# Performance work log

Hardware: AMD Instinct MI355X
Metric: run time of the kernel (lower is better)

## Reference

```python
import jax, jax.numpy as jnp
import numpy as np

KSIZE = 3  # module init kwarg


def setup_inputs() -> dict:
    key = jax.random.key(0)
    k1, k2, k3 = jax.random.split(key, 3)
    shape = (16, 3, 512, 512)  # [B, C, H, W]
    return {
        "sr": jax.random.normal(k1, shape, jnp.float32),
        "sr_ema": jax.random.normal(k2, shape, jnp.float32),
        "hr": jax.random.normal(k3, shape, jnp.float32),
    }


def _local_var(res, ksize):
    """Unbiased variance over a ksize x ksize sliding window with reflect pad.

    Matches torch: reflect-pad then unfold + var(unbiased=True). Implemented as a
    box-filter over sum and sum-of-squares (no ksize^2-larger unfold tensor).
    res: [B, 1, H, W] -> [B, 1, H, W]
    """
    pad = (ksize - 1) // 2
    rp = jnp.pad(res, ((0, 0), (0, 0), (pad, pad), (pad, pad)), mode="reflect")
    n = ksize * ksize
    win = (1, 1, ksize, ksize)
    strides = (1, 1, 1, 1)
    zero = jnp.zeros((), rp.dtype)
    s = jax.lax.reduce_window(rp, zero, jax.lax.add, win, strides, "VALID")
    sq = jax.lax.reduce_window(rp * rp, zero, jax.lax.add, win, strides, "VALID")
    # unbiased: (sum(x^2) - sum(x)^2/n) / (n-1)
    return (sq - s * s / n) / (n - 1)


def reference(sr, sr_ema, hr):
    # per-pixel channel-summed residuals, [B, 1, H, W]
    residual_ema = jnp.sum(jnp.abs(hr - sr_ema), axis=1, keepdims=True) / 255.0
    residual_sr = jnp.sum(jnp.abs(hr - sr), axis=1, keepdims=True) / 255.0

    r_det = jax.lax.stop_gradient(residual_sr)  # .clone().detach() in torch

    # patch-level weight: unbiased var over (C=1, H, W) per sample, ** (1/5)
    n_patch = r_det.shape[1] * r_det.shape[2] * r_det.shape[3]
    mean = jnp.mean(r_det, axis=(-1, -2, -3), keepdims=True)
    patch_var = jnp.sum((r_det - mean) ** 2, axis=(-1, -2, -3), keepdims=True) / (n_patch - 1)
    patch_w = patch_var ** 0.2  # [B,1,1,1]

    pixel_w = _local_var(r_det, KSIZE)  # [B,1,H,W]

    overall_w = patch_w * pixel_w
    overall_w = jnp.where(residual_sr < residual_ema, jnp.zeros((), overall_w.dtype), overall_w)

    # L1 loss (mean reduction) between weighted sr and weighted hr
    return jnp.mean(jnp.abs(overall_w * sr - overall_w * hr))
```

## Files before the change

kernel.cpp:

```cpp
#include <hip/hip_runtime.h>
#include <math.h>


#define BB 16
#define HH 512
#define WW 512
#define HW (HH * WW)
#define CHW (3 * HW)
#define TILES_PER_BATCH 64
#define NBLOCKS (BB * TILES_PER_BATCH)
#define LDS_STRIDE 264

__device__ __forceinline__ int reflect_h(int gh) {
  gh = gh < 0 ? -gh : gh;
  return gh >= HH ? 2 * HH - 2 - gh : gh;
}

__global__ __launch_bounds__(256, 4) void wl1_main(
    const float* __restrict__ sr, const float* __restrict__ srema,
    const float* __restrict__ hr,
    float* __restrict__ p_sum, float* __restrict__ p_sum2,
    float* __restrict__ p_loss) {
  __shared__ float rt[18][LDS_STRIDE];
  const int bid = blockIdx.x;
  const int b = bid >> 6;
  const int t = bid & 63;
  const int h0 = (t >> 1) << 4;
  const int w0 = (t & 1) << 8;
  const int tid = threadIdx.x;
  const int c4 = tid & 63;
  const int rs = tid >> 6;
  const float* __restrict__ srb = sr + (size_t)b * CHW;
  const float* __restrict__ hrb = hr + (size_t)b * CHW;
  const float* __restrict__ eb = srema + (size_t)b * CHW;

  if (tid < 36) {
    int row = tid >> 1, side = tid & 1;
    int gh = reflect_h(h0 - 1 + row);
    int gw = side ? w0 + 256 : w0 - 1;
    if (gw < 0) gw = 1;
    if (gw > 511) gw = 1022 - gw;
    int base = gh * WW + gw;
    float v = (fabsf(hrb[base] - srb[base]) +
               fabsf(hrb[base + HW] - srb[base + HW]) +
               fabsf(hrb[base + 2 * HW] - srb[base + 2 * HW])) /
              255.0f;
    rt[row][side ? 260 : 3] = v;
  }

  float e_r[4][4];
#pragma unroll
  for (int it = 0; it < 5; ++it) {
    const int row = 4 * it + rs;
    if (row < 18) {
      const int gh = reflect_h(h0 - 1 + row);
      const float* hb = hrb + gh * WW + w0 + 4 * c4;
      const float* sb = srb + gh * WW + w0 + 4 * c4;
      float4 ha = *(const float4*)(hb);
      float4 hbv = *(const float4*)(hb + HW);
      float4 hc = *(const float4*)(hb + 2 * HW);
      float4 sa = *(const float4*)(sb);
      float4 sbv = *(const float4*)(sb + HW);
      float4 sc = *(const float4*)(sb + 2 * HW);
      const bool do_e = (row >= 1) && (row <= 16);
      float4 ea, eb2, ec;
      if (do_e) {
        const float* ep = eb + gh * WW + w0 + 4 * c4;
        ea = *(const float4*)(ep);
        eb2 = *(const float4*)(ep + HW);
        ec = *(const float4*)(ep + 2 * HW);
      }
      float4 r4;
      r4.x = (fabsf(ha.x - sa.x) + fabsf(hbv.x - sbv.x) + fabsf(hc.x - sc.x)) / 255.0f;
      r4.y = (fabsf(ha.y - sa.y) + fabsf(hbv.y - sbv.y) + fabsf(hc.y - sc.y)) / 255.0f;
      r4.z = (fabsf(ha.z - sa.z) + fabsf(hbv.z - sbv.z) + fabsf(hc.z - sc.z)) / 255.0f;
      r4.w = (fabsf(ha.w - sa.w) + fabsf(hbv.w - sbv.w) + fabsf(hc.w - sc.w)) / 255.0f;
      *(float4*)&rt[row][4 + 4 * c4] = r4;
      if (do_e) {
        e_r[it & 3][0] = (fabsf(ha.x - ea.x) + fabsf(hbv.x - eb2.x) + fabsf(hc.x - ec.x)) / 255.0f;
        e_r[it & 3][1] = (fabsf(ha.y - ea.y) + fabsf(hbv.y - eb2.y) + fabsf(hc.y - ec.y)) / 255.0f;
        e_r[it & 3][2] = (fabsf(ha.z - ea.z) + fabsf(hbv.z - eb2.z) + fabsf(hc.z - ec.z)) / 255.0f;
        e_r[it & 3][3] = (fabsf(ha.w - ea.w) + fabsf(hbv.w - eb2.w) + fabsf(hc.w - ec.w)) / 255.0f;
      }
    }
  }
  __syncthreads();

  float v1 = 0.f, v2 = 0.f, v3 = 0.f;
#pragma unroll
  for (int it = 0; it < 5; ++it) {
    const int row = 4 * it + rs;
    if (row >= 1 && row <= 16) {
      const int o = row - 1;
      float cs[6] = {0, 0, 0, 0, 0, 0}, cq[6] = {0, 0, 0, 0, 0, 0};
      float center[4];
#pragma unroll
      for (int dr = 0; dr < 3; ++dr) {
        const float* lp = &rt[o + dr][4 * c4];
        float4 a = *(const float4*)(lp);
        float4 bq = *(const float4*)(lp + 4);
        float4 cq4 = *(const float4*)(lp + 8);
        float f3 = a.w, f4 = bq.x, f5 = bq.y, f6 = bq.z, f7 = bq.w, f8 = cq4.x;
        cs[0] += f3; cq[0] += f3 * f3;
        cs[1] += f4; cq[1] += f4 * f4;
        cs[2] += f5; cq[2] += f5 * f5;
        cs[3] += f6; cq[3] += f6 * f6;
        cs[4] += f7; cq[4] += f7 * f7;
        cs[5] += f8; cq[5] += f8 * f8;
        if (dr == 1) { center[0] = f4; center[1] = f5; center[2] = f6; center[3] = f7; }
      }
#pragma unroll
      for (int cc = 0; cc < 4; ++cc) {
        float s = cs[cc] + cs[cc + 1] + cs[cc + 2];
        float q = cq[cc] + cq[cc + 1] + cq[cc + 2];
        float pvar = (q - s * s / 9.0f) / 8.0f;
        float rc = center[cc];
        v1 += rc;
        v2 += rc * rc;
        if (rc >= e_r[it & 3][cc]) v3 += pvar * (255.0f * rc);
      }
    }
  }

#pragma unroll
  for (int off = 32; off > 0; off >>= 1) {
    v1 += __shfl_down(v1, off, 64);
    v2 += __shfl_down(v2, off, 64);
    v3 += __shfl_down(v3, off, 64);
  }
  __shared__ float red[3][4];
  if (c4 == 0) {
    red[0][rs] = v1;
    red[1][rs] = v2;
    red[2][rs] = v3;
  }
  __syncthreads();
  if (tid == 0) {
    p_sum[bid] = red[0][0] + red[0][1] + red[0][2] + red[0][3];
    p_sum2[bid] = red[1][0] + red[1][1] + red[1][2] + red[1][3];
    p_loss[bid] = red[2][0] + red[2][1] + red[2][2] + red[2][3];
  }
}

__global__ __launch_bounds__(1024) void wl1_reduce(
    const float* __restrict__ p_sum, const float* __restrict__ p_sum2,
    const float* __restrict__ p_loss, float* __restrict__ out) {
  const int tid = threadIdx.x;
  const int b = tid >> 6, k = tid & 63;
  const int i = b * TILES_PER_BATCH + k;
  double s = (double)p_sum[i], s2 = (double)p_sum2[i], sl = (double)p_loss[i];
#pragma unroll
  for (int off = 32; off > 0; off >>= 1) {
    s += __shfl_down(s, off, 64);
    s2 += __shfl_down(s2, off, 64);
    sl += __shfl_down(sl, off, 64);
  }
  __shared__ double acc[BB];
  if (k == 0) {
    const double n = (double)HW;
    double var = (s2 - s * s / n) / (n - 1.0);
    acc[b] = pow(var, 0.2) * sl;
  }
  __syncthreads();
  if (tid == 0) {
    double tot = 0.0;
#pragma unroll
    for (int j = 0; j < BB; ++j) tot += acc[j];
    out[0] = (float)(tot / (double)((size_t)BB * CHW));
  }
}

extern "C" void kernel_launch(void* const* d_in, const int* in_sizes, int n_in,
                              void* d_out, int out_size, void* d_ws,
                              size_t ws_size, hipStream_t stream) {
  const float* sr = (const float*)d_in[0];
  const float* srema = (const float*)d_in[1];
  const float* hr = (const float*)d_in[2];
  float* out = (float*)d_out;

  float* p_sum = (float*)d_ws;
  float* p_sum2 = p_sum + NBLOCKS;
  float* p_loss = p_sum2 + NBLOCKS;

  wl1_main<<<NBLOCKS, 256, 0, stream>>>(sr, srema, hr, p_sum, p_sum2, p_loss);
  wl1_reduce<<<1, 1024, 0, stream>>>(p_sum, p_sum2, p_loss, out);
}
```

Baseline: 167.8 us.

## Replace LDS tile with per-wave register rolling window over row strips

Each wave now processes an 8-row, 256-column strip, streaming rows through registers with a prefetched next row and a rolling three-row window of box-filter partial sums. Horizontal neighbours come from lane shuffles, so the shared-memory tile and its block barrier are gone. Halo reread overhead rises (2 extra rows per 8 instead of per 16), and register pressure grows, which is why launch bounds drop to two blocks per CU. The reduce kernel is adjusted for 32 blocks per batch.

```diff
diff --git a/kernel.cpp b/kernel.cpp
--- a/kernel.cpp
+++ b/kernel.cpp
@@ -7,119 +7,145 @@
 #define WW 512
 #define HW (HH * WW)
 #define CHW (3 * HW)
-#define TILES_PER_BATCH 64
-#define NBLOCKS (BB * TILES_PER_BATCH)
-#define LDS_STRIDE 264
+#define SH 8
+#define STRIPS (HH / SH)
+#define BLOCKS_PER_BATCH ((STRIPS * 2) / 4)
+#define NBLOCKS (BB * BLOCKS_PER_BATCH)
 
 __device__ __forceinline__ int reflect_h(int gh) {
   gh = gh < 0 ? -gh : gh;
   return gh >= HH ? 2 * HH - 2 - gh : gh;
 }
 
-__global__ __launch_bounds__(256, 4) void wl1_main(
+struct Row {
+  float4 h0, h1, h2, s0, s1, s2, m0, m1, m2;
+  float eh0, eh1, eh2, es0, es1, es2;
+};
+
+__device__ __forceinline__ Row load_row(const float* __restrict__ hrb,
+                                        const float* __restrict__ srb,
+                                        const float* __restrict__ emb,
+                                        int gh, int col, bool isEdge, int gwE,
+                                        bool with_e) {
+  Row r;
+  const int base = gh * WW + col;
+  r.h0 = *(const float4*)(hrb + base);
+  r.h1 = *(const float4*)(hrb + base + HW);
+  r.h2 = *(const float4*)(hrb + base + 2 * HW);
+  r.s0 = *(const float4*)(srb + base);
+  r.s1 = *(const float4*)(srb + base + HW);
+  r.s2 = *(const float4*)(srb + base + 2 * HW);
+  if (with_e) {
+    r.m0 = *(const float4*)(emb + base);
+    r.m1 = *(const float4*)(emb + base + HW);
+    r.m2 = *(const float4*)(emb + base + 2 * HW);
+  }
+  if (isEdge) {
+    const int be = gh * WW + gwE;
+    r.eh0 = hrb[be];
+    r.eh1 = hrb[be + HW];
+    r.eh2 = hrb[be + 2 * HW];
+    r.es0 = srb[be];
+    r.es1 = srb[be + HW];
+    r.es2 = srb[be + 2 * HW];
+  }
+  return r;
+}
+
+__global__ __launch_bounds__(256, 2) void wl1_main(
     const float* __restrict__ sr, const float* __restrict__ srema,
     const float* __restrict__ hr,
     float* __restrict__ p_sum, float* __restrict__ p_sum2,
     float* __restrict__ p_loss) {
-  __shared__ float rt[18][LDS_STRIDE];
+  const int tid = threadIdx.x;
+  const int wv = tid >> 6;
+  const int lane = tid & 63;
   const int bid = blockIdx.x;
-  const int b = bid >> 6;
-  const int t = bid & 63;
-  const int h0 = (t >> 1) << 4;
-  const int w0 = (t & 1) << 8;
-  const int tid = threadIdx.x;
-  const int c4 = tid & 63;
-  const int rs = tid >> 6;
+  const int b = bid >> 5;
+  const int slot = ((bid & 31) << 2) | wv;
+  const int r0 = (slot >> 1) * SH;
+  const int w0 = (slot & 1) << 8;
+  const int col = w0 + 4 * lane;
+  const bool isEdge = (lane == 0) || (lane == 63);
+  const int gwE = (lane == 0) ? (w0 ? w0 - 1 : 1)
+                              : (w0 + 256 < WW ? w0 + 256 : 2 * WW - 2 - (w0 + 256));
   const float* __restrict__ srb = sr + (size_t)b * CHW;
   const float* __restrict__ hrb = hr + (size_t)b * CHW;
-  const float* __restrict__ eb = srema + (size_t)b * CHW;
-
-  if (tid < 36) {
-    int row = tid >> 1, side = tid & 1;
-    int gh = reflect_h(h0 - 1 + row);
-    int gw = side ? w0 + 256 : w0 - 1;
-    if (gw < 0) gw = 1;
-    if (gw > 511) gw = 1022 - gw;
-    int base = gh * WW + gw;
-    float v = (fabsf(hrb[base] - srb[base]) +
-               fabsf(hrb[base + HW] - srb[base + HW]) +
-               fabsf(hrb[base + 2 * HW] - srb[base + 2 * HW])) /
-              255.0f;
-    rt[row][side ? 260 : 3] = v;
-  }
-
-  float e_r[4][4];
-#pragma unroll
-  for (int it = 0; it < 5; ++it) {
-    const int row = 4 * it + rs;
-    if (row < 18) {
-      const int gh = reflect_h(h0 - 1 + row);
-      const float* hb = hrb + gh * WW + w0 + 4 * c4;
-      const float* sb = srb + gh * WW + w0 + 4 * c4;
-      float4 ha = *(const float4*)(hb);
-      float4 hbv = *(const float4*)(hb + HW);
-      float4 hc = *(const float4*)(hb + 2 * HW);
-      float4 sa = *(const float4*)(sb);
-      float4 sbv = *(const float4*)(sb + HW);
-      float4 sc = *(const float4*)(sb + 2 * HW);
-      const bool do_e = (row >= 1) && (row <= 16);
-      float4 ea, eb2, ec;
-      if (do_e) {
-        const float* ep = eb + gh * WW + w0 + 4 * c4;
-        ea = *(const float4*)(ep);
-        eb2 = *(const float4*)(ep + HW);
-        ec = *(const float4*)(ep + 2 * HW);
-      }
-      float4 r4;
-      r4.x = (fabsf(ha.x - sa.x) + fabsf(hbv.x - sbv.x) + fabsf(hc.x - sc.x)) / 255.0f;
-      r4.y = (fabsf(ha.y - sa.y) + fabsf(hbv.y - sbv.y) + fabsf(hc.y - sc.y)) / 255.0f;
-      r4.z = (fabsf(ha.z - sa.z) + fabsf(hbv.z - sbv.z) + fabsf(hc.z - sc.z)) / 255.0f;
-      r4.w = (fabsf(ha.w - sa.w) + fabsf(hbv.w - sbv.w) + fabsf(hc.w - sc.w)) / 255.0f;
-      *(float4*)&rt[row][4 + 4 * c4] = r4;
-      if (do_e) {
-        e_r[it & 3][0] = (fabsf(ha.x - ea.x) + fabsf(hbv.x - eb2.x) + fabsf(hc.x - ec.x)) / 255.0f;
-        e_r[it & 3][1] = (fabsf(ha.y - ea.y) + fabsf(hbv.y - eb2.y) + fabsf(hc.y - ec.y)) / 255.0f;
-        e_r[it & 3][2] = (fabsf(ha.z - ea.z) + fabsf(hbv.z - eb2.z) + fabsf(hc.z - ec.z)) / 255.0f;
-        e_r[it & 3][3] = (fabsf(ha.w - ea.w) + fabsf(hbv.w - eb2.w) + fabsf(hc.w - ec.w)) / 255.0f;
-      }
-    }
-  }
-  __syncthreads();
-
+  const float* __restrict__ emb = srema + (size_t)b * CHW;
+
+  float hA[4] = {0, 0, 0, 0}, qA[4] = {0, 0, 0, 0};
+  float hB[4] = {0, 0, 0, 0}, qB[4] = {0, 0, 0, 0};
+  float cB[4] = {0, 0, 0, 0}, eB[4] = {0, 0, 0, 0};
   float v1 = 0.f, v2 = 0.f, v3 = 0.f;
-#pragma unroll
-  for (int it = 0; it < 5; ++it) {
-    const int row = 4 * it + rs;
-    if (row >= 1 && row <= 16) {
-      const int o = row - 1;
-      float cs[6] = {0, 0, 0, 0, 0, 0}, cq[6] = {0, 0, 0, 0, 0, 0};
-      float center[4];
-#pragma unroll
-      for (int dr = 0; dr < 3; ++dr) {
-        const float* lp = &rt[o + dr][4 * c4];
-        float4 a = *(const float4*)(lp);
-        float4 bq = *(const float4*)(lp + 4);
-        float4 cq4 = *(const float4*)(lp + 8);
-        float f3 = a.w, f4 = bq.x, f5 = bq.y, f6 = bq.z, f7 = bq.w, f8 = cq4.x;
-        cs[0] += f3; cq[0] += f3 * f3;
-        cs[1] += f4; cq[1] += f4 * f4;
-        cs[2] += f5; cq[2] += f5 * f5;
-        cs[3] += f6; cq[3] += f6 * f6;
-        cs[4] += f7; cq[4] += f7 * f7;
-        cs[5] += f8; cq[5] += f8 * f8;
-        if (dr == 1) { center[0] = f4; center[1] = f5; center[2] = f6; center[3] = f7; }
-      }
+
+  Row cur = load_row(hrb, srb, emb, reflect_h(r0 - 1), col, isEdge, gwE, false);
+#pragma unroll
+  for (int st = 0; st <= SH + 1; ++st) {
+    Row nxt;
+    if (st <= SH) {
+      const int gh1 = (st == SH) ? reflect_h(r0 + SH) : (r0 + st);
+      nxt = load_row(hrb, srb, emb, gh1, col, isEdge, gwE, st < SH);
+    }
+    float4 r4;
+    r4.x = (fabsf(cur.h0.x - cur.s0.x) + fabsf(cur.h1.x - cur.s1.x) +
+            fabsf(cur.h2.x - cur.s2.x)) / 255.0f;
+    r4.y = (fabsf(cur.h0.y - cur.s0.y) + fabsf(cur.h1.y - cur.s1.y) +
+            fabsf(cur.h2.y - cur.s2.y)) / 255.0f;
+    r4.z = (fabsf(cur.h0.z - cur.s0.z) + fabsf(cur.h1.z - cur.s1.z) +
+            fabsf(cur.h2.z - cur.s2.z)) / 255.0f;
+    r4.w = (fabsf(cur.h0.w - cur.s0.w) + fabsf(cur.h1.w - cur.s1.w) +
+            fabsf(cur.h2.w - cur.s2.w)) / 255.0f;
+    float redge = 0.f;
+    if (isEdge)
+      redge = (fabsf(cur.eh0 - cur.es0) + fabsf(cur.eh1 - cur.es1) +
+               fabsf(cur.eh2 - cur.es2)) / 255.0f;
+    const float fl = __shfl_up(r4.w, 1, 64);
+    const float fr = __shfl_down(r4.x, 1, 64);
+    const float f3 = (lane == 0) ? redge : fl;
+    const float f8 = (lane == 63) ? redge : fr;
+    const float f0 = f3, f1v = r4.x, f2v = r4.y, f3v = r4.z, f4v = r4.w, f5v = f8;
+    float hC[4], qC[4];
+    hC[0] = f0 + f1v + f2v;
+    hC[1] = f1v + f2v + f3v;
+    hC[2] = f2v + f3v + f4v;
+    hC[3] = f3v + f4v + f5v;
+    qC[0] = f0 * f0 + f1v * f1v + f2v * f2v;
+    qC[1] = f1v * f1v + f2v * f2v + f3v * f3v;
+    qC[2] = f2v * f2v + f3v * f3v + f4v * f4v;
+    qC[3] = f3v * f3v + f4v * f4v + f5v * f5v;
+    float e4[4] = {0, 0, 0, 0};
+    if (st >= 1 && st <= SH) {
+      e4[0] = (fabsf(cur.h0.x - cur.m0.x) + fabsf(cur.h1.x - cur.m1.x) +
+               fabsf(cur.h2.x - cur.m2.x)) / 255.0f;
+      e4[1] = (fabsf(cur.h0.y - cur.m0.y) + fabsf(cur.h1.y - cur.m1.y) +
+               fabsf(cur.h2.y - cur.m2.y)) / 255.0f;
+      e4[2] = (fabsf(cur.h0.z - cur.m0.z) + fabsf(cur.h1.z - cur.m1.z) +
+               fabsf(cur.h2.z - cur.m2.z)) / 255.0f;
+      e4[3] = (fabsf(cur.h0.w - cur.m0.w) + fabsf(cur.h1.w - cur.m1.w) +
+               fabsf(cur.h2.w - cur.m2.w)) / 255.0f;
+    }
+    if (st >= 2) {
 #pragma unroll
       for (int cc = 0; cc < 4; ++cc) {
-        float s = cs[cc] + cs[cc + 1] + cs[cc + 2];
-        float q = cq[cc] + cq[cc + 1] + cq[cc + 2];
-        float pvar = (q - s * s / 9.0f) / 8.0f;
-        float rc = center[cc];
+        const float s3 = hA[cc] + hB[cc] + hC[cc];
+        const float q3 = qA[cc] + qB[cc] + qC[cc];
+        const float pvar = (q3 - s3 * s3 / 9.0f) / 8.0f;
+        const float rc = cB[cc];
         v1 += rc;
         v2 += rc * rc;
-        if (rc >= e_r[it & 3][cc]) v3 += pvar * (255.0f * rc);
+        if (rc >= eB[cc]) v3 += pvar * (255.0f * rc);
       }
     }
+#pragma unroll
+    for (int cc = 0; cc < 4; ++cc) {
+      hA[cc] = hB[cc];
+      qA[cc] = qB[cc];
+      hB[cc] = hC[cc];
+      qB[cc] = qC[cc];
+    }
+    cB[0] = r4.x; cB[1] = r4.y; cB[2] = r4.z; cB[3] = r4.w;
+    eB[0] = e4[0]; eB[1] = e4[1]; eB[2] = e4[2]; eB[3] = e4[3];
+    cur = nxt;
   }
 
 #pragma unroll
@@ -129,10 +155,10 @@
     v3 += __shfl_down(v3, off, 64);
   }
   __shared__ float red[3][4];
-  if (c4 == 0) {
-    red[0][rs] = v1;
-    red[1][rs] = v2;
-    red[2][rs] = v3;
+  if (lane == 0) {
+    red[0][wv] = v1;
+    red[1][wv] = v2;
+    red[2][wv] = v3;
   }
   __syncthreads();
   if (tid == 0) {
@@ -147,8 +173,13 @@
     const float* __restrict__ p_loss, float* __restrict__ out) {
   const int tid = threadIdx.x;
   const int b = tid >> 6, k = tid & 63;
-  const int i = b * TILES_PER_BATCH + k;
-  double s = (double)p_sum[i], s2 = (double)p_sum2[i], sl = (double)p_loss[i];
+  double s = 0.0, s2 = 0.0, sl = 0.0;
+  if (k < BLOCKS_PER_BATCH) {
+    const int i = b * BLOCKS_PER_BATCH + k;
+    s = (double)p_sum[i];
+    s2 = (double)p_sum2[i];
+    sl = (double)p_loss[i];
+  }
 #pragma unroll
   for (int off = 32; off > 0; off >>= 1) {
     s += __shfl_down(s, off, 64);
```

New measurement: 172.3 us. 2.7% more time.

## Fuse final reduction into main kernel via last-block atomic counter

Applied to the files above, without the earlier changes.

Merges the separate reduction kernel into the main kernel: each block bumps an atomic counter after writing its partials, and the last block does the per-batch variance and final sum. The load phase is also restructured. Interior rows are loaded with full sr/sr_ema/hr and the ema residual is stashed in LDS, while the two halo rows go to 128 dedicated threads. Patch sums move into the load loop. The change removes one kernel launch and the register array, but adds a memset, an atomic with fences, and a dead leftover loop that sums partials nobody uses.

```diff
diff --git a/kernel.cpp b/kernel.cpp
--- a/kernel.cpp
+++ b/kernel.cpp
@@ -7,8 +7,7 @@
 #define WW 512
 #define HW (HH * WW)
 #define CHW (3 * HW)
-#define TILES_PER_BATCH 64
-#define NBLOCKS (BB * TILES_PER_BATCH)
+#define NT 1024
 #define LDS_STRIDE 264
 
 __device__ __forceinline__ int reflect_h(int gh) {
@@ -16,12 +15,14 @@
   return gh >= HH ? 2 * HH - 2 - gh : gh;
 }
 
-__global__ __launch_bounds__(256, 4) void wl1_main(
+__global__ __launch_bounds__(256) void wl1_fused(
     const float* __restrict__ sr, const float* __restrict__ srema,
     const float* __restrict__ hr,
     float* __restrict__ p_sum, float* __restrict__ p_sum2,
-    float* __restrict__ p_loss) {
+    float* __restrict__ p_loss, unsigned int* __restrict__ counter,
+    float* __restrict__ out) {
   __shared__ float rt[18][LDS_STRIDE];
+  __shared__ float ee[16][256];
   const int bid = blockIdx.x;
   const int b = bid >> 6;
   const int t = bid & 63;
@@ -32,93 +33,105 @@
   const int rs = tid >> 6;
   const float* __restrict__ srb = sr + (size_t)b * CHW;
   const float* __restrict__ hrb = hr + (size_t)b * CHW;
-  const float* __restrict__ eb = srema + (size_t)b * CHW;
-
-  if (tid < 36) {
-    int row = tid >> 1, side = tid & 1;
-    int gh = reflect_h(h0 - 1 + row);
+  const float* __restrict__ emb = srema + (size_t)b * CHW;
+
+  float v1 = 0.f, v2 = 0.f, v3 = 0.f;
+
+#pragma unroll
+  for (int k = 0; k < 4; ++k) {
+    const int o = 4 * k + rs;
+    const int base = (h0 + o) * WW + w0 + 4 * c4;
+    const float* hp = hrb + base;
+    const float* sp = srb + base;
+    const float* ep = emb + base;
+    float4 h0v = *(const float4*)(hp);
+    float4 h1v = *(const float4*)(hp + HW);
+    float4 h2v = *(const float4*)(hp + 2 * HW);
+    float4 s0v = *(const float4*)(sp);
+    float4 s1v = *(const float4*)(sp + HW);
+    float4 s2v = *(const float4*)(sp + 2 * HW);
+    float4 e0v = *(const float4*)(ep);
+    float4 e1v = *(const float4*)(ep + HW);
+    float4 e2v = *(const float4*)(ep + 2 * HW);
+    float4 r4;
+    r4.x = (fabsf(h0v.x - s0v.x) + fabsf(h1v.x - s1v.x) + fabsf(h2v.x - s2v.x)) / 255.0f;
+    r4.y = (fabsf(h0v.y - s0v.y) + fabsf(h1v.y - s1v.y) + fabsf(h2v.y - s2v.y)) / 255.0f;
+    r4.z = (fabsf(h0v.z - s0v.z) + fabsf(h1v.z - s1v.z) + fabsf(h2v.z - s2v.z)) / 255.0f;
+    r4.w = (fabsf(h0v.w - s0v.w) + fabsf(h1v.w - s1v.w) + fabsf(h2v.w - s2v.w)) / 255.0f;
+    float4 e4;
+    e4.x = (fabsf(h0v.x - e0v.x) + fabsf(h1v.x - e1v.x) + fabsf(h2v.x - e2v.x)) / 255.0f;
+    e4.y = (fabsf(h0v.y - e0v.y) + fabsf(h1v.y - e1v.y) + fabsf(h2v.y - e2v.y)) / 255.0f;
+    e4.z = (fabsf(h0v.z - e0v.z) + fabsf(h1v.z - e1v.z) + fabsf(h2v.z - e2v.z)) / 255.0f;
+    e4.w = (fabsf(h0v.w - e0v.w) + fabsf(h1v.w - e1v.w) + fabsf(h2v.w - e2v.w)) / 255.0f;
+    *(float4*)&rt[o + 1][4 + 4 * c4] = r4;
+    *(float4*)&ee[o][4 * c4] = e4;
+    v1 += r4.x + r4.y + r4.z + r4.w;
+    v2 += r4.x * r4.x + r4.y * r4.y + r4.z * r4.z + r4.w * r4.w;
+  }
+
+  if (tid < 128) {
+    const int row = (tid >> 6) * 17;
+    const int gh = reflect_h(h0 - 1 + row);
+    const int base = gh * WW + w0 + 4 * (tid & 63);
+    const float* hp = hrb + base;
+    const float* sp = srb + base;
+    float4 h0v = *(const float4*)(hp);
+    float4 h1v = *(const float4*)(hp + HW);
+    float4 h2v = *(const float4*)(hp + 2 * HW);
+    float4 s0v = *(const float4*)(sp);
+    float4 s1v = *(const float4*)(sp + HW);
+    float4 s2v = *(const float4*)(sp + 2 * HW);
+    float4 r4;
+    r4.x = (fabsf(h0v.x - s0v.x) + fabsf(h1v.x - s1v.x) + fabsf(h2v.x - s2v.x)) / 255.0f;
+    r4.y = (fabsf(h0v.y - s0v.y) + fabsf(h1v.y - s1v.y) + fabsf(h2v.y - s2v.y)) / 255.0f;
+    r4.z = (fabsf(h0v.z - s0v.z) + fabsf(h1v.z - s1v.z) + fabsf(h2v.z - s2v.z)) / 255.0f;
+    r4.w = (fabsf(h0v.w - s0v.w) + fabsf(h1v.w - s1v.w) + fabsf(h2v.w - s2v.w)) / 255.0f;
+    *(float4*)&rt[row][4 + 4 * (tid & 63)] = r4;
+  } else if (tid < 164) {
+    const int ht = tid - 128;
+    const int row = ht >> 1, side = ht & 1;
+    const int gh = reflect_h(h0 - 1 + row);
     int gw = side ? w0 + 256 : w0 - 1;
     if (gw < 0) gw = 1;
     if (gw > 511) gw = 1022 - gw;
-    int base = gh * WW + gw;
+    const int base = gh * WW + gw;
     float v = (fabsf(hrb[base] - srb[base]) +
                fabsf(hrb[base + HW] - srb[base + HW]) +
                fabsf(hrb[base + 2 * HW] - srb[base + 2 * HW])) /
               255.0f;
     rt[row][side ? 260 : 3] = v;
   }
-
-  float e_r[4][4];
-#pragma unroll
-  for (int it = 0; it < 5; ++it) {
-    const int row = 4 * it + rs;
-    if (row < 18) {
-      const int gh = reflect_h(h0 - 1 + row);
-      const float* hb = hrb + gh * WW + w0 + 4 * c4;
-      const float* sb = srb + gh * WW + w0 + 4 * c4;
-      float4 ha = *(const float4*)(hb);
-      float4 hbv = *(const float4*)(hb + HW);
-      float4 hc = *(const float4*)(hb + 2 * HW);
-      float4 sa = *(const float4*)(sb);
-      float4 sbv = *(const float4*)(sb + HW);
-      float4 sc = *(const float4*)(sb + 2 * HW);
-      const bool do_e = (row >= 1) && (row <= 16);
-      float4 ea, eb2, ec;
-      if (do_e) {
-        const float* ep = eb + gh * WW + w0 + 4 * c4;
-        ea = *(const float4*)(ep);
-        eb2 = *(const float4*)(ep + HW);
-        ec = *(const float4*)(ep + 2 * HW);
-      }
-      float4 r4;
-      r4.x = (fabsf(ha.x - sa.x) + fabsf(hbv.x - sbv.x) + fabsf(hc.x - sc.x)) / 255.0f;
-      r4.y = (fabsf(ha.y - sa.y) + fabsf(hbv.y - sbv.y) + fabsf(hc.y - sc.y)) / 255.0f;
-      r4.z = (fabsf(ha.z - sa.z) + fabsf(hbv.z - sbv.z) + fabsf(hc.z - sc.z)) / 255.0f;
-      r4.w = (fabsf(ha.w - sa.w) + fabsf(hbv.w - sbv.w) + fabsf(hc.w - sc.w)) / 255.0f;
-      *(float4*)&rt[row][4 + 4 * c4] = r4;
-      if (do_e) {
-        e_r[it & 3][0] = (fabsf(ha.x - ea.x) + fabsf(hbv.x - eb2.x) + fabsf(hc.x - ec.x)) / 255.0f;
-        e_r[it & 3][1] = (fabsf(ha.y - ea.y) + fabsf(hbv.y - eb2.y) + fabsf(hc.y - ec.y)) / 255.0f;
-        e_r[it & 3][2] = (fabsf(ha.z - ea.z) + fabsf(hbv.z - eb2.z) + fabsf(hc.z - ec.z)) / 255.0f;
-        e_r[it & 3][3] = (fabsf(ha.w - ea.w) + fabsf(hbv.w - eb2.w) + fabsf(hc.w - ec.w)) / 255.0f;
-      }
-    }
-  }
-  __syncthreads();
-
-  float v1 = 0.f, v2 = 0.f, v3 = 0.f;
-#pragma unroll
-  for (int it = 0; it < 5; ++it) {
-    const int row = 4 * it + rs;
-    if (row >= 1 && row <= 16) {
-      const int o = row - 1;
-      float cs[6] = {0, 0, 0, 0, 0, 0}, cq[6] = {0, 0, 0, 0, 0, 0};
-      float center[4];
-#pragma unroll
-      for (int dr = 0; dr < 3; ++dr) {
-        const float* lp = &rt[o + dr][4 * c4];
-        float4 a = *(const float4*)(lp);
-        float4 bq = *(const float4*)(lp + 4);
-        float4 cq4 = *(const float4*)(lp + 8);
-        float f3 = a.w, f4 = bq.x, f5 = bq.y, f6 = bq.z, f7 = bq.w, f8 = cq4.x;
-        cs[0] += f3; cq[0] += f3 * f3;
-        cs[1] += f4; cq[1] += f4 * f4;
-        cs[2] += f5; cq[2] += f5 * f5;
-        cs[3] += f6; cq[3] += f6 * f6;
-        cs[4] += f7; cq[4] += f7 * f7;
-        cs[5] += f8; cq[5] += f8 * f8;
-        if (dr == 1) { center[0] = f4; center[1] = f5; center[2] = f6; center[3] = f7; }
-      }
-#pragma unroll
-      for (int cc = 0; cc < 4; ++cc) {
-        float s = cs[cc] + cs[cc + 1] + cs[cc + 2];
-        float q = cq[cc] + cq[cc + 1] + cq[cc + 2];
-        float pvar = (q - s * s / 9.0f) / 8.0f;
-        float rc = center[cc];
-        v1 += rc;
-        v2 += rc * rc;
-        if (rc >= e_r[it & 3][cc]) v3 += pvar * (255.0f * rc);
-      }
+  __syncthreads();
+
+#pragma unroll
+  for (int rr = 0; rr < 4; ++rr) {
+    const int o = 4 * rr + rs;
+    float cs[6] = {0, 0, 0, 0, 0, 0}, cq[6] = {0, 0, 0, 0, 0, 0};
+    float center[4];
+#pragma unroll
+    for (int dr = 0; dr < 3; ++dr) {
+      const float* lp = &rt[o + dr][4 * c4];
+      float4 a = *(const float4*)(lp);
+      float4 bq = *(const float4*)(lp + 4);
+      float4 cq4 = *(const float4*)(lp + 8);
+      float f3 = a.w, f4 = bq.x, f5 = bq.y, f6 = bq.z, f7 = bq.w, f8 = cq4.x;
+      cs[0] += f3; cq[0] += f3 * f3;
+      cs[1] += f4; cq[1] += f4 * f4;
+      cs[2] += f5; cq[2] += f5 * f5;
+      cs[3] += f6; cq[3] += f6 * f6;
+      cs[4] += f7; cq[4] += f7 * f7;
+      cs[5] += f8; cq[5] += f8 * f8;
+      if (dr == 1) { center[0] = f4; center[1] = f5; center[2] = f6; center[3] = f7; }
+    }
+    const float4 e4 = *(const float4*)&ee[o][4 * c4];
+    const float ev[4] = {e4.x, e4.y, e4.z, e4.w};
+#pragma unroll
+    for (int cc = 0; cc < 4; ++cc) {
+      float s = cs[cc] + cs[cc + 1] + cs[cc + 2];
+      float q = cq[cc] + cq[cc + 1] + cq[cc + 2];
+      float pvar = (q - s * s / 9.0f) / 8.0f;
+      float rc = center[cc];
+      if (rc >= ev[cc]) v3 += pvar * (255.0f * rc);
     }
   }
 
@@ -135,37 +148,60 @@
     red[2][rs] = v3;
   }
   __syncthreads();
+  __shared__ int is_last;
   if (tid == 0) {
     p_sum[bid] = red[0][0] + red[0][1] + red[0][2] + red[0][3];
     p_sum2[bid] = red[1][0] + red[1][1] + red[1][2] + red[1][3];
     p_loss[bid] = red[2][0] + red[2][1] + red[2][2] + red[2][3];
-  }
-}
-
-__global__ __launch_bounds__(1024) void wl1_reduce(
-    const float* __restrict__ p_sum, const float* __restrict__ p_sum2,
-    const float* __restrict__ p_loss, float* __restrict__ out) {
-  const int tid = threadIdx.x;
-  const int b = tid >> 6, k = tid & 63;
-  const int i = b * TILES_PER_BATCH + k;
-  double s = (double)p_sum[i], s2 = (double)p_sum2[i], sl = (double)p_loss[i];
-#pragma unroll
-  for (int off = 32; off > 0; off >>= 1) {
-    s += __shfl_down(s, off, 64);
-    s2 += __shfl_down(s2, off, 64);
-    sl += __shfl_down(sl, off, 64);
-  }
-  __shared__ double acc[BB];
-  if (k == 0) {
-    const double n = (double)HW;
-    double var = (s2 - s * s / n) / (n - 1.0);
-    acc[b] = pow(var, 0.2) * sl;
+    __threadfence();
+    unsigned int prev = atomicAdd(counter, 1u);
+    is_last = (prev == NT - 1) ? 1 : 0;
+  }
+  __syncthreads();
+  if (is_last == 0) return;
+
+  __threadfence();
+  double s = 0.0, s2 = 0.0, sl = 0.0;
+#pragma unroll
+  for (int j = 0; j < 4; ++j) {
+    const int i = tid + 256 * j;
+    s += (double)p_sum[i];
+    s2 += (double)p_sum2[i];
+    sl += (double)p_loss[i];
+  }
+  __shared__ double bs[BB], bs2[BB], bsl[BB];
+  if (tid < BB) { bs[tid] = 0.0; bs2[tid] = 0.0; bsl[tid] = 0.0; }
+  __syncthreads();
+  if (tid < 64) {
+  }
+  if (tid < 128) {
+    const int bb = tid >> 3;
+    const int kk = tid & 7;
+    double ls = 0.0, ls2 = 0.0, lsl = 0.0;
+#pragma unroll
+    for (int j = 0; j < 8; ++j) {
+      const int i = (bb << 6) + (kk << 3) + j;
+      ls += (double)p_sum[i];
+      ls2 += (double)p_sum2[i];
+      lsl += (double)p_loss[i];
+    }
+#pragma unroll
+    for (int off = 4; off > 0; off >>= 1) {
+      ls += __shfl_down(ls, off, 64);
+      ls2 += __shfl_down(ls2, off, 64);
+      lsl += __shfl_down(lsl, off, 64);
+    }
+    if (kk == 0) {
+      const double n = (double)HW;
+      double var = (ls2 - ls * ls / n) / (n - 1.0);
+      bs[bb] = pow(var, 0.2) * lsl;
+    }
   }
   __syncthreads();
   if (tid == 0) {
     double tot = 0.0;
 #pragma unroll
-    for (int j = 0; j < BB; ++j) tot += acc[j];
+    for (int j = 0; j < BB; ++j) tot += bs[j];
     out[0] = (float)(tot / (double)((size_t)BB * CHW));
   }
 }
@@ -179,9 +215,11 @@
   float* out = (float*)d_out;
 
   float* p_sum = (float*)d_ws;
-  float* p_sum2 = p_sum + NBLOCKS;
-  float* p_loss = p_sum2 + NBLOCKS;
-
-  wl1_main<<<NBLOCKS, 256, 0, stream>>>(sr, srema, hr, p_sum, p_sum2, p_loss);
-  wl1_reduce<<<1, 1024, 0, stream>>>(p_sum, p_sum2, p_loss, out);
+  float* p_sum2 = p_sum + NT;
+  float* p_loss = p_sum2 + NT;
+  unsigned int* counter = (unsigned int*)(p_loss + NT);
+
+  hipMemsetAsync(counter, 0, sizeof(unsigned int), stream);
+  wl1_fused<<<NT, 256, 0, stream>>>(sr, srema, hr, p_sum, p_sum2, p_loss,
+                                    counter, out);
 }
```

Result: slower. 206.7 us (+23.2%).
